# Kernel optimization log

Measured on AMD Instinct MI355X. Metric: run time of the kernel, lower is better.

Reference implementation:

```python
import jax, jax.numpy as jnp
import numpy as np

DIM, H, KV, HD, WIN = 1024, 16, 4, 64, 512
EPS = 1e-6


def rmsnorm(x, w, eps=EPS):
    # torch.nn.RMSNorm: x * rsqrt(mean(x^2, -1) + eps) * w
    return x * jax.lax.rsqrt(jnp.mean(x * x, axis=-1, keepdims=True) + eps) * w


def setup_inputs() -> dict:
    key = jax.random.key(0)
    ks = jax.random.split(key, 7)
    B, T = 4, 2048
    s = 0.02
    return {
        "x": jax.random.normal(ks[0], (B, T, DIM), dtype=jnp.float32),
        "wq": jax.random.normal(ks[1], (H * HD, DIM), dtype=jnp.float32) * s,
        "wk": jax.random.normal(ks[2], (KV * HD, DIM), dtype=jnp.float32) * s,
        "wv": jax.random.normal(ks[3], (KV * HD, DIM), dtype=jnp.float32) * s,
        "wo": jax.random.normal(ks[4], (DIM, H * HD), dtype=jnp.float32) * s,
        "q_norm_w": jnp.ones((HD,), dtype=jnp.float32),
        "k_norm_w": jnp.ones((HD,), dtype=jnp.float32),
    }


def reference(x, wq, wk, wv, wo, q_norm_w, k_norm_w):
    B, T, D = x.shape
    rep = H // KV
    q = (x @ wq.T).reshape(B, T, H, HD)
    k = (x @ wk.T).reshape(B, T, KV, HD)
    v = (x @ wv.T).reshape(B, T, KV, HD)
    q = rmsnorm(q, q_norm_w)
    k = rmsnorm(k, k_norm_w)
    # GQA repeat: each kv head repeated `rep` times contiguously
    k = jnp.repeat(k, rep, axis=2)  # [B,T,H,HD]
    v = jnp.repeat(v, rep, axis=2)
    # scores [B,H,T,T]
    scores = jnp.einsum('bqhd,bkhd->bhqk', q, k) / jnp.sqrt(jnp.float32(HD))
    i = jnp.arange(T)[:, None]
    j = jnp.arange(T)[None, :]
    mask = (i >= j) & (i - j < WIN)  # causal sliding window band
    scores = jnp.where(mask, scores, -jnp.inf)
    attn = jax.nn.softmax(scores, axis=-1)
    y = jnp.einsum('bhqk,bkhd->bqhd', attn, v).reshape(B, T, H * HD)
    return y @ wo.T
```

## Files before the change

### kernel.cpp

```cpp
#include <hip/hip_runtime.h>
#include <hip/hip_bf16.h>

#define DIMD 1024
#define NH   16
#define NKV  4
#define HDIM 64
#define WINSZ 512
#define BB   4
#define TT   2048
#define MROWS (BB*TT)
#define NQKV 1536

typedef __attribute__((ext_vector_type(8))) short short8;
typedef __attribute__((ext_vector_type(4))) float f32x4;

static __device__ __forceinline__ short f2bf(float f) {
  __hip_bfloat16 h = __float2bfloat16(f);
  return __builtin_bit_cast(short, h);
}
static __device__ __forceinline__ float bf2f(short s) {
  return __bfloat162float(__builtin_bit_cast(__hip_bfloat16, s));
}
static __device__ __forceinline__ unsigned pk2(float a, float b) {
  unsigned lo = (unsigned short)f2bf(a);
  unsigned hi = (unsigned short)f2bf(b);
  return lo | (hi << 16);
}

static __device__ __forceinline__ void gld_lds16(const void* g, void* l) {
  __builtin_amdgcn_global_load_lds(
      (const __attribute__((address_space(1))) unsigned int*)g,
      (__attribute__((address_space(3))) unsigned int*)l, 16, 0, 0);
}

template<int N>
static __device__ __forceinline__ float dpp_ror(float x) {
  return __builtin_bit_cast(float, __builtin_amdgcn_update_dpp(
      0, __builtin_bit_cast(int, x), 0x120 + N, 0xF, 0xF, true));
}

__global__ __launch_bounds__(256) void cvt_all_kernel(
    const float* __restrict__ x, const float* __restrict__ wq,
    const float* __restrict__ wk, const float* __restrict__ wv,
    const float* __restrict__ wo,
    short* __restrict__ xb, short* __restrict__ wqkvb, short* __restrict__ wob) {
  size_t u = (size_t)blockIdx.x * 256 + threadIdx.x;
  const float* src; short* dst;
  if (u < 2097152)                   { src = x;  dst = xb; }
  else if ((u -= 2097152) < 262144)  { src = wq; dst = wqkvb; }
  else if ((u -= 262144) < 65536)    { src = wk; dst = wqkvb + 1024*1024; }
  else if ((u -= 65536) < 65536)     { src = wv; dst = wqkvb + 1280*1024; }
  else { u -= 65536;                   src = wo; dst = wob; }
  float4 v = ((const float4*)src)[u];
  short4 o;
  o.x = f2bf(v.x); o.y = f2bf(v.y); o.z = f2bf(v.z); o.w = f2bf(v.w);
  ((short4*)dst)[u] = o;
}

#define BMT 128
#define BNT 128
#define BKT 64

template<bool OUT_BF16>
__global__ __launch_bounds__(256) void gemm_bt(
    const short* __restrict__ A, const short* __restrict__ Bw,
    void* __restrict__ Cout, int M, int N, int K) {
  __shared__ __align__(16) short As[BMT*BKT];
  __shared__ __align__(16) short Bs[BNT*BKT];

  int nwg  = gridDim.x;
  int orig = blockIdx.x;
  int wg   = (orig & 7) * (nwg >> 3) + (orig >> 3);
  int tiles_n = N / BNT;
  int m0 = (wg / tiles_n) * BMT;
  int n0 = (wg % tiles_n) * BNT;

  int tid = threadIdx.x;
  int lane = tid & 63, wv = tid >> 6;
  int l15 = lane & 15, lg = lane >> 4;
  int wr = wv >> 1, wc = wv & 1;

  f32x4 acc[4][4] = {};

  for (int k0 = 0; k0 < K; k0 += BKT) {
    __syncthreads();
    const char* Abase = (const char*)(A + (size_t)m0 * K + k0);
    const char* Bbase = (const char*)(Bw + (size_t)n0 * K + k0);
#pragma unroll
    for (int i = 0; i < 4; ++i) {
      int idx = i * 256 + tid;
      int row = idx >> 3;
      int cb  = (idx & 7) << 4;
      int scb = cb ^ ((row & 7) << 4);
      gld_lds16(Abase + (size_t)row * (K * 2) + scb,
                (char*)As + ((i * 256 + wv * 64) << 4));
      gld_lds16(Bbase + (size_t)row * (K * 2) + scb,
                (char*)Bs + ((i * 256 + wv * 64) << 4));
    }
    __syncthreads();

#pragma unroll
    for (int kk = 0; kk < 2; ++kk) {
      short8 af[4], bfr[4];
      int kb = (kk * 32 + lg * 8) * 2;
#pragma unroll
      for (int mi = 0; mi < 4; ++mi) {
        int row = wr * 64 + mi * 16 + l15;
        af[mi] = *(const short8*)((const char*)As + row * 128 + (kb ^ ((row & 7) << 4)));
      }
#pragma unroll
      for (int ni = 0; ni < 4; ++ni) {
        int row = wc * 64 + ni * 16 + l15;
        bfr[ni] = *(const short8*)((const char*)Bs + row * 128 + (kb ^ ((row & 7) << 4)));
      }
#pragma unroll
      for (int mi = 0; mi < 4; ++mi)
#pragma unroll
        for (int ni = 0; ni < 4; ++ni)
          acc[mi][ni] = __builtin_amdgcn_mfma_f32_16x16x32_bf16(af[mi], bfr[ni], acc[mi][ni], 0, 0, 0);
    }
  }

  int crow0 = m0 + wr * 64, ccol0 = n0 + wc * 64;
#pragma unroll
  for (int mi = 0; mi < 4; ++mi)
#pragma unroll
    for (int ni = 0; ni < 4; ++ni)
#pragma unroll
      for (int r = 0; r < 4; ++r) {
        int row = crow0 + mi * 16 + lg * 4 + r;
        int col = ccol0 + ni * 16 + l15;
        float v = acc[mi][ni][r];
        if (OUT_BF16) ((short*)Cout)[(size_t)row * N + col] = f2bf(v);
        else          ((float*)Cout)[(size_t)row * N + col] = v;
      }
}

__global__ __launch_bounds__(256) void qk_norm_kernel(
    const short* __restrict__ qkv, const float* __restrict__ qw,
    const float* __restrict__ kw, short* __restrict__ Qh, short* __restrict__ Kh) {
  unsigned gid = blockIdx.x * 16u + (threadIdx.x >> 4);
  int l = threadIdx.x & 15;
  unsigned row = gid / 20u;
  int s = (int)(gid - row * 20u);
  int b = row >> 11, t = row & 2047;
  bool isq = s < 16;
  int col = isq ? s * 64 : 1024 + (s - 16) * 64;
  const short* rp = qkv + (size_t)row * NQKV + col + l * 4;
  short4 v4 = *(const short4*)rp;
  float f0 = bf2f(v4.x), f1 = bf2f(v4.y), f2 = bf2f(v4.z), f3 = bf2f(v4.w);
  float ss = f0 * f0 + f1 * f1 + f2 * f2 + f3 * f3;
  ss += dpp_ror<1>(ss); ss += dpp_ror<2>(ss);
  ss += dpp_ror<4>(ss); ss += dpp_ror<8>(ss);
  float r = rsqrtf(ss * (1.0f / 64.0f) + 1e-6f);
  float4 w4 = *(const float4*)((isq ? qw : kw) + l * 4);
  short4 o;
  o.x = f2bf(f0 * r * w4.x); o.y = f2bf(f1 * r * w4.y);
  o.z = f2bf(f2 * r * w4.z); o.w = f2bf(f3 * r * w4.w);
  if (isq) *(short4*)(Qh + (((size_t)b * NH + s) * TT + t) * HDIM + l * 4) = o;
  else     *(short4*)(Kh + (((size_t)b * NKV + (s - 16)) * TT + t) * HDIM + l * 4) = o;
}

__global__ __launch_bounds__(256) void vtrans_kernel(
    const short* __restrict__ qkv, short* __restrict__ Vt) {
  int tb = blockIdx.x, kv = blockIdx.y, b = blockIdx.z;
  __shared__ short tile[64][72];
  int tid = threadIdx.x;
#pragma unroll
  for (int i = 0; i < 2; ++i) {
    int idx = i * 256 + tid;
    int tr = idx >> 3;
    int c8 = (idx & 7) * 8;
    int t = tb * 64 + tr;
    const short* src = qkv + (size_t)(b * TT + t) * NQKV + 1280 + kv * 64 + c8;
    short8 v = *(const short8*)src;
#pragma unroll
    for (int j = 0; j < 8; ++j) tile[tr][c8 + j] = v[j];
  }
  __syncthreads();
#pragma unroll
  for (int i = 0; i < 2; ++i) {
    int idx = i * 256 + tid;
    int d = idx >> 3;
    int t8 = (idx & 7) * 8;
    short8 o;
#pragma unroll
    for (int j = 0; j < 8; ++j) o[j] = tile[t8 + j][d];
    short* dst = Vt + (((size_t)(b * NKV + kv) * HDIM) + d) * TT + tb * 64 + t8;
    *(short8*)dst = o;
  }
}

#define C1A 0.180336880f
#define C2A 11.5415603f

__global__ __launch_bounds__(256) void attn_kernel(
    const short* __restrict__ Qh, const short* __restrict__ Kh,
    const short* __restrict__ Vt, short* __restrict__ Y) {
  int wgid = blockIdx.x;
  int qh = wgid >> 4;
  int kvh = (wgid >> 2) & 3;
  int b = wgid & 3;
  int tid = threadIdx.x, lane = tid & 63, wv = tid >> 6;
  int l15 = lane & 15, lg = lane >> 4;
  int h = kvh * 4 + wv;
  int q0 = qh * 32;
  const short* Qp = Qh + (((size_t)b * NH + h) * TT + q0) * HDIM;
  const char*  Kp = (const char*)(Kh + ((size_t)b * NKV + kvh) * TT * HDIM);
  const short* Vp = Vt + ((size_t)b * NKV + kvh) * HDIM * TT;

  short8 aqA0 = *(const short8*)(Qp + l15 * HDIM + lg * 8);
  short8 aqA1 = *(const short8*)(Qp + l15 * HDIM + 32 + lg * 8);
  short8 aqB0 = *(const short8*)(Qp + (16 + l15) * HDIM + lg * 8);
  short8 aqB1 = *(const short8*)(Qp + (16 + l15) * HDIM + 32 + lg * 8);

  float lpA = 0.f, lpB = 0.f;
  f32x4 yA[4] = {}, yB[4] = {};

  __shared__ __align__(16) char smem[26624];
  char* Kbuf = smem;
  short* PA = (short*)(smem + 8192 + wv * 4608);
  short* PB = PA + 1152;

  int lo = q0 - (WINSZ - 1); if (lo < 0) lo = 0;
  int klo = lo & ~63;
  int nt = (q0 + 32 - klo + 63) >> 6;

  int qiA = q0 + l15, qiB = qiA + 16;

  for (int t = 0; t < nt; ++t) {
    int kc = klo + t * 64;
    __syncthreads();
#pragma unroll
    for (int r = 0; r < 2; ++r) {
      int rr = wv * 16 + r * 8 + (lane >> 3);
      int cb = (lane & 7) * 16;
      gld_lds16(Kp + (size_t)(kc + rr) * 128 + (cb ^ ((rr & 7) << 4)),
                Kbuf + wv * 2048 + r * 1024);
    }
    __syncthreads();

    short8 bv0[4], bv1[4];
#pragma unroll
    for (int dt = 0; dt < 4; ++dt) {
      const short* vb = Vp + (size_t)(dt * 16 + l15) * TT + kc + lg * 8;
      bv0[dt] = *(const short8*)vb;
      bv1[dt] = *(const short8*)(vb + 32);
    }
    short8 bk0[4], bk1[4];
    int sw = (l15 & 7) << 4;
#pragma unroll
    for (int nc = 0; nc < 4; ++nc) {
      int rb = (nc * 16 + l15) * 128;
      bk0[nc] = *(const short8*)(Kbuf + rb + ((lg * 16) ^ sw));
      bk1[nc] = *(const short8*)(Kbuf + rb + ((lg * 16 + 64) ^ sw));
    }
    f32x4 sA[4], sB[4];
    __builtin_amdgcn_s_setprio(1);
#pragma unroll
    for (int nc = 0; nc < 4; ++nc) {
      f32x4 zA = {}, zB = {};
      zA = __builtin_amdgcn_mfma_f32_16x16x32_bf16(bk0[nc], aqA0, zA, 0, 0, 0);
      zB = __builtin_amdgcn_mfma_f32_16x16x32_bf16(bk0[nc], aqB0, zB, 0, 0, 0);
      zA = __builtin_amdgcn_mfma_f32_16x16x32_bf16(bk1[nc], aqA1, zA, 0, 0, 0);
      zB = __builtin_amdgcn_mfma_f32_16x16x32_bf16(bk1[nc], aqB1, zB, 0, 0, 0);
      sA[nc] = zA; sB[nc] = zB;
    }
    __builtin_amdgcn_s_setprio(0);
    bool intA = (kc >= q0 - 496) && (kc + 63 <= q0);
    bool intB = (kc >= q0 - 480) && (kc + 63 <= q0 + 16);
    if (intA && intB) {
#pragma unroll
      for (int nc = 0; nc < 4; ++nc) {
        float pa0 = __builtin_amdgcn_exp2f(fmaf(sA[nc][0], C1A, -C2A));
        float pa1 = __builtin_amdgcn_exp2f(fmaf(sA[nc][1], C1A, -C2A));
        float pa2 = __builtin_amdgcn_exp2f(fmaf(sA[nc][2], C1A, -C2A));
        float pa3 = __builtin_amdgcn_exp2f(fmaf(sA[nc][3], C1A, -C2A));
        float pb0 = __builtin_amdgcn_exp2f(fmaf(sB[nc][0], C1A, -C2A));
        float pb1 = __builtin_amdgcn_exp2f(fmaf(sB[nc][1], C1A, -C2A));
        float pb2 = __builtin_amdgcn_exp2f(fmaf(sB[nc][2], C1A, -C2A));
        float pb3 = __builtin_amdgcn_exp2f(fmaf(sB[nc][3], C1A, -C2A));
        lpA += (pa0 + pa1) + (pa2 + pa3);
        lpB += (pb0 + pb1) + (pb2 + pb3);
        *(uint2*)(PA + l15 * 72 + nc * 16 + lg * 4) = uint2{pk2(pa0, pa1), pk2(pa2, pa3)};
        *(uint2*)(PB + l15 * 72 + nc * 16 + lg * 4) = uint2{pk2(pb0, pb1), pk2(pb2, pb3)};
      }
    } else {
      int kjb = kc + lg * 4;
#pragma unroll
      for (int nc = 0; nc < 4; ++nc) {
        float pa[4], pb[4];
#pragma unroll
        for (int r = 0; r < 4; ++r) {
          int kj = kjb + nc * 16 + r;
          bool okA = (kj <= qiA) && (qiA - kj < WINSZ);
          bool okB = (kj <= qiB) && (qiB - kj < WINSZ);
          pa[r] = okA ? __builtin_amdgcn_exp2f(fmaf(sA[nc][r], C1A, -C2A)) : 0.f;
          pb[r] = okB ? __builtin_amdgcn_exp2f(fmaf(sB[nc][r], C1A, -C2A)) : 0.f;
        }
        lpA += (pa[0] + pa[1]) + (pa[2] + pa[3]);
        lpB += (pb[0] + pb[1]) + (pb[2] + pb[3]);
        *(uint2*)(PA + l15 * 72 + nc * 16 + lg * 4) = uint2{pk2(pa[0], pa[1]), pk2(pa[2], pa[3])};
        *(uint2*)(PB + l15 * 72 + nc * 16 + lg * 4) = uint2{pk2(pb[0], pb[1]), pk2(pb[2], pb[3])};
      }
    }
    short8 apA0 = *(const short8*)(PA + l15 * 72 + lg * 8);
    short8 apA1 = *(const short8*)(PA + l15 * 72 + 32 + lg * 8);
    short8 apB0 = *(const short8*)(PB + l15 * 72 + lg * 8);
    short8 apB1 = *(const short8*)(PB + l15 * 72 + 32 + lg * 8);
    __builtin_amdgcn_s_setprio(1);
#pragma unroll
    for (int dt = 0; dt < 4; ++dt) {
      yA[dt] = __builtin_amdgcn_mfma_f32_16x16x32_bf16(apA0, bv0[dt], yA[dt], 0, 0, 0);
      yB[dt] = __builtin_amdgcn_mfma_f32_16x16x32_bf16(apB0, bv0[dt], yB[dt], 0, 0, 0);
      yA[dt] = __builtin_amdgcn_mfma_f32_16x16x32_bf16(apA1, bv1[dt], yA[dt], 0, 0, 0);
      yB[dt] = __builtin_amdgcn_mfma_f32_16x16x32_bf16(apB1, bv1[dt], yB[dt], 0, 0, 0);
    }
    __builtin_amdgcn_s_setprio(0);
  }

  lpA += __shfl_xor(lpA, 16); lpA += __shfl_xor(lpA, 32);
  lpB += __shfl_xor(lpB, 16); lpB += __shfl_xor(lpB, 32);
  float invqA = 1.0f / lpA;
  float invqB = 1.0f / lpB;
#pragma unroll
  for (int r = 0; r < 4; ++r) {
    float invA = __builtin_bit_cast(float, __builtin_amdgcn_ds_bpermute(
        (lg * 4 + r) << 2, __builtin_bit_cast(int, invqA)));
    float invB = __builtin_bit_cast(float, __builtin_amdgcn_ds_bpermute(
        (lg * 4 + r) << 2, __builtin_bit_cast(int, invqB)));
    int qiAo = q0 + lg * 4 + r, qiBo = qiAo + 16;
#pragma unroll
    for (int dt = 0; dt < 4; ++dt) {
      Y[((size_t)(b * TT + qiAo)) * DIMD + h * HDIM + dt * 16 + l15] = f2bf(yA[dt][r] * invA);
      Y[((size_t)(b * TT + qiBo)) * DIMD + h * HDIM + dt * 16 + l15] = f2bf(yB[dt][r] * invB);
    }
  }
}

extern "C" void kernel_launch(void* const* d_in, const int* in_sizes, int n_in,
                              void* d_out, int out_size, void* d_ws, size_t ws_size,
                              hipStream_t stream) {
  const float* x  = (const float*)d_in[0];
  const float* wq = (const float*)d_in[1];
  const float* wk = (const float*)d_in[2];
  const float* wv = (const float*)d_in[3];
  const float* wo = (const float*)d_in[4];
  const float* qw = (const float*)d_in[5];
  const float* kw = (const float*)d_in[6];

  char* ws = (char*)d_ws;
  short* xb    = (short*)(ws + 0);
  short* wqkvb = (short*)(ws + 16777216);
  short* wob   = (short*)(ws + 19922944);
  short* qkv   = (short*)(ws + 22020096);
  short* Qh    = (short*)(ws + 47185920);
  short* Kh    = (short*)(ws + 63963136);
  short* Vt    = (short*)(ws + 68157440);
  short* Y     = xb;
  float* outp  = (float*)d_out;

  cvt_all_kernel<<<10752, 256, 0, stream>>>(x, wq, wk, wv, wo, xb, wqkvb, wob);
  gemm_bt<true><<<dim3(64 * 12), 256, 0, stream>>>(xb, wqkvb, (void*)qkv, MROWS, NQKV, DIMD);
  qk_norm_kernel<<<10240, 256, 0, stream>>>(qkv, qw, kw, Qh, Kh);
  vtrans_kernel<<<dim3(32, 4, 4), 256, 0, stream>>>(qkv, Vt);
  attn_kernel<<<1024, 256, 0, stream>>>(Qh, Kh, Vt, Y);
  gemm_bt<false><<<dim3(64 * 8), 256, 0, stream>>>(Y, wob, (void*)outp, MROWS, DIMD, DIMD);
}
```

Measured before the change: 130.5 us.

## Split attention key range across two wave groups per block

Doubles the attention block to 512 threads, with the second set of four waves processing the second half of the key tiles for the same query rows. Partial outputs and row sums are combined through shared memory at the end. This targets latency and occupancy in the attention kernel, where each block used to walk up to nine key tiles in sequence. In exchange it doubles LDS use, adds a reduction step, and leaves waves idle when the tile count is odd. It relies on a fixed exponent offset rather than a running max, so the unnormalized partial sums can simply be added.

```diff
diff --git a/kernel.cpp b/kernel.cpp
--- a/kernel.cpp
+++ b/kernel.cpp
@@ -194,7 +194,7 @@
 #define C1A 0.180336880f
 #define C2A 11.5415603f
 
-__global__ __launch_bounds__(256) void attn_kernel(
+__global__ __launch_bounds__(512) void attn_kernel(
     const short* __restrict__ Qh, const short* __restrict__ Kh,
     const short* __restrict__ Vt, short* __restrict__ Y) {
   int wgid = blockIdx.x;
@@ -202,8 +202,9 @@
   int kvh = (wgid >> 2) & 3;
   int b = wgid & 3;
   int tid = threadIdx.x, lane = tid & 63, wv = tid >> 6;
+  int head = wv & 3, khalf = wv >> 2;
   int l15 = lane & 15, lg = lane >> 4;
-  int h = kvh * 4 + wv;
+  int h = kvh * 4 + head;
   int q0 = qh * 32;
   const short* Qp = Qh + (((size_t)b * NH + h) * TT + q0) * HDIM;
   const char*  Kp = (const char*)(Kh + ((size_t)b * NKV + kvh) * TT * HDIM);
@@ -217,28 +218,35 @@
   float lpA = 0.f, lpB = 0.f;
   f32x4 yA[4] = {}, yB[4] = {};
 
-  __shared__ __align__(16) char smem[26624];
+  __shared__ __align__(16) char smem[53248];
   char* Kbuf = smem;
-  short* PA = (short*)(smem + 8192 + wv * 4608);
+  short* PA = (short*)(smem + 16384 + wv * 4608);
   short* PB = PA + 1152;
 
   int lo = q0 - (WINSZ - 1); if (lo < 0) lo = 0;
   int klo = lo & ~63;
   int nt = (q0 + 32 - klo + 63) >> 6;
+  int tmid = (nt + 1) >> 1;
 
   int qiA = q0 + l15, qiB = qiA + 16;
-
-  for (int t = 0; t < nt; ++t) {
-    int kc = klo + t * 64;
+  const char* kbase = Kbuf + khalf * 8192;
+
+  for (int it = 0; it < tmid; ++it) {
+    int tmine = it + khalf * tmid;
+    bool valid = tmine < nt;
+    int kc = klo + tmine * 64;
     __syncthreads();
-#pragma unroll
-    for (int r = 0; r < 2; ++r) {
-      int rr = wv * 16 + r * 8 + (lane >> 3);
-      int cb = (lane & 7) * 16;
-      gld_lds16(Kp + (size_t)(kc + rr) * 128 + (cb ^ ((rr & 7) << 4)),
-                Kbuf + wv * 2048 + r * 1024);
+    if (valid) {
+#pragma unroll
+      for (int r = 0; r < 2; ++r) {
+        int rr = head * 16 + r * 8 + (lane >> 3);
+        int cb = (lane & 7) * 16;
+        gld_lds16(Kp + (size_t)(kc + rr) * 128 + (cb ^ ((rr & 7) << 4)),
+                  Kbuf + khalf * 8192 + head * 2048 + r * 1024);
+      }
     }
     __syncthreads();
+    if (!valid) continue;
 
     short8 bv0[4], bv1[4];
 #pragma unroll
@@ -252,8 +260,8 @@
 #pragma unroll
     for (int nc = 0; nc < 4; ++nc) {
       int rb = (nc * 16 + l15) * 128;
-      bk0[nc] = *(const short8*)(Kbuf + rb + ((lg * 16) ^ sw));
-      bk1[nc] = *(const short8*)(Kbuf + rb + ((lg * 16 + 64) ^ sw));
+      bk0[nc] = *(const short8*)(kbase + rb + ((lg * 16) ^ sw));
+      bk1[nc] = *(const short8*)(kbase + rb + ((lg * 16 + 64) ^ sw));
     }
     f32x4 sA[4], sB[4];
     __builtin_amdgcn_s_setprio(1);
@@ -321,19 +329,42 @@
 
   lpA += __shfl_xor(lpA, 16); lpA += __shfl_xor(lpA, 32);
   lpB += __shfl_xor(lpB, 16); lpB += __shfl_xor(lpB, 32);
-  float invqA = 1.0f / lpA;
-  float invqB = 1.0f / lpB;
-#pragma unroll
-  for (int r = 0; r < 4; ++r) {
-    float invA = __builtin_bit_cast(float, __builtin_amdgcn_ds_bpermute(
-        (lg * 4 + r) << 2, __builtin_bit_cast(int, invqA)));
-    float invB = __builtin_bit_cast(float, __builtin_amdgcn_ds_bpermute(
-        (lg * 4 + r) << 2, __builtin_bit_cast(int, invqB)));
-    int qiAo = q0 + lg * 4 + r, qiBo = qiAo + 16;
+
+  __syncthreads();
+  f32x4* ybuf = (f32x4*)(smem + 16384 + head * 8192);
+  float* lbufA = (float*)(smem + 16384 + 32768 + head * 128);
+  float* lbufB = lbufA + 16;
+  if (khalf) {
 #pragma unroll
     for (int dt = 0; dt < 4; ++dt) {
-      Y[((size_t)(b * TT + qiAo)) * DIMD + h * HDIM + dt * 16 + l15] = f2bf(yA[dt][r] * invA);
-      Y[((size_t)(b * TT + qiBo)) * DIMD + h * HDIM + dt * 16 + l15] = f2bf(yB[dt][r] * invB);
+      ybuf[dt * 64 + lane] = yA[dt];
+      ybuf[(4 + dt) * 64 + lane] = yB[dt];
+    }
+    if (lg == 0) { lbufA[l15] = lpA; lbufB[l15] = lpB; }
+  }
+  __syncthreads();
+  if (!khalf) {
+#pragma unroll
+    for (int dt = 0; dt < 4; ++dt) {
+      f32x4 pa = ybuf[dt * 64 + lane];
+      f32x4 pb = ybuf[(4 + dt) * 64 + lane];
+#pragma unroll
+      for (int r = 0; r < 4; ++r) { yA[dt][r] += pa[r]; yB[dt][r] += pb[r]; }
+    }
+    float invqA = 1.0f / (lpA + lbufA[l15]);
+    float invqB = 1.0f / (lpB + lbufB[l15]);
+#pragma unroll
+    for (int r = 0; r < 4; ++r) {
+      float invA = __builtin_bit_cast(float, __builtin_amdgcn_ds_bpermute(
+          (lg * 4 + r) << 2, __builtin_bit_cast(int, invqA)));
+      float invB = __builtin_bit_cast(float, __builtin_amdgcn_ds_bpermute(
+          (lg * 4 + r) << 2, __builtin_bit_cast(int, invqB)));
+      int qiAo = q0 + lg * 4 + r, qiBo = qiAo + 16;
+#pragma unroll
+      for (int dt = 0; dt < 4; ++dt) {
+        Y[((size_t)(b * TT + qiAo)) * DIMD + h * HDIM + dt * 16 + l15] = f2bf(yA[dt][r] * invA);
+        Y[((size_t)(b * TT + qiBo)) * DIMD + h * HDIM + dt * 16 + l15] = f2bf(yB[dt][r] * invB);
+      }
     }
   }
 }
@@ -364,6 +395,6 @@
   gemm_bt<true><<<dim3(64 * 12), 256, 0, stream>>>(xb, wqkvb, (void*)qkv, MROWS, NQKV, DIMD);
   qk_norm_kernel<<<10240, 256, 0, stream>>>(qkv, qw, kw, Qh, Kh);
   vtrans_kernel<<<dim3(32, 4, 4), 256, 0, stream>>>(qkv, Vt);
-  attn_kernel<<<1024, 256, 0, stream>>>(Qh, Kh, Vt, Y);
+  attn_kernel<<<1024, 512, 0, stream>>>(Qh, Kh, Vt, Y);
   gemm_bt<false><<<dim3(64 * 8), 256, 0, stream>>>(Y, wob, (void*)outp, MROWS, DIMD, DIMD);
 }
```

New measurement: 131.4 us. About the same (+0.7%).
